# Performance work log

Measured on AMD Instinct MI355X. Metric: run time of the kernel, lower is better.

## Reference

```python
import jax, jax.numpy as jnp
import numpy as np


def binarize(t):
    # sign binarizer to exactly +/-1 (sign(0) -> +1), matching is_binary_tensor check
    return jnp.where(t >= 0, 1.0, -1.0).astype(t.dtype)


def setup_inputs() -> dict:
    key = jax.random.key(0)
    kx, kw, kb = jax.random.split(key, 3)
    x = jax.random.normal(kx, (32, 256, 56, 56), dtype=jnp.float32)
    weight = jax.random.normal(kw, (256, 256, 3, 3), dtype=jnp.float32)
    bias = jax.random.normal(kb, (256,), dtype=jnp.float32)
    return {"x": x, "weight": weight, "bias": bias}


def reference(x, weight, bias):
    bx = binarize(x)            # [B, Cin, H, W] in {-1, +1}
    bw = binarize(weight)       # [Cout, Cin, kh, kw] in {-1, +1}
    # F.conv2d(stride=1, padding=1, dilation=1, groups=1)
    out = jax.lax.conv_general_dilated(
        bx, bw,
        window_strides=(1, 1),
        padding=((1, 1), (1, 1)),
        dimension_numbers=("NCHW", "OIHW", "NCHW"),
    )
    return out + bias[None, :, None, None]
```

## Files before the change

kernel.cpp:

```cpp
#include <hip/hip_runtime.h>
#include <cstdint>

constexpr int B = 32, C = 256, H = 56, W = 56;
constexpr int HW = H * W;
constexpr int WORDS = C / 32;
constexpr int TAPS = 9;
constexpr int WPC = TAPS * WORDS;

__global__ __launch_bounds__(256) void pack_x_kernel(const float* __restrict__ x,
                                                     uint32_t* __restrict__ px) {
    int idx = blockIdx.x * 256 + threadIdx.x;
    if (idx >= B * HW) return;
    int b = idx / HW;
    int hw = idx - b * HW;
    const float* xp = x + (size_t)b * C * HW + hw;
    uint32_t words[WORDS];
    for (int wd = 0; wd < WORDS; ++wd) {
        uint32_t bits = 0;
        #pragma unroll
        for (int i = 0; i < 32; ++i) {
            bits |= (xp[(size_t)(wd * 32 + i) * HW] < 0.0f ? (1u << i) : 0u);
        }
        words[wd] = bits;
    }
    uint4* dst = reinterpret_cast<uint4*>(px + (size_t)idx * WORDS);
    dst[0] = make_uint4(words[0], words[1], words[2], words[3]);
    dst[1] = make_uint4(words[4], words[5], words[6], words[7]);
}

__global__ __launch_bounds__(256) void pack_w_kernel(const float* __restrict__ wt,
                                                     uint32_t* __restrict__ pw) {
    int idx = blockIdx.x * 256 + threadIdx.x;
    if (idx >= C * WPC) return;
    int co = idx / WPC;
    int r = idx - co * WPC;
    int tap = r / WORDS;
    int wd = r - tap * WORDS;
    const float* wp = wt + ((size_t)co * C + wd * 32) * TAPS + tap;
    uint32_t bits = 0;
    #pragma unroll
    for (int i = 0; i < 32; ++i)
        bits |= (wp[(size_t)i * TAPS] < 0.0f ? (1u << i) : 0u);
    pw[(size_t)co * WPC + (size_t)tap * WORDS + wd] = bits;
}

__global__ __launch_bounds__(64) void bconv_kernel(const uint32_t* __restrict__ px,
                                                   const uint32_t* __restrict__ pw,
                                                   const float* __restrict__ bias,
                                                   float* __restrict__ out) {
    const int lane = threadIdx.x;
    const int hw = blockIdx.x * 64 + lane;
    const int cobase = blockIdx.y * 64;
    const int b = blockIdx.z;
    const int h = hw / W;
    const int w = hw - h * W;

    uint32_t pxr[TAPS][WORDS];
    bool valid[TAPS];
    int nvalid = 0;
    #pragma unroll
    for (int dh = -1; dh <= 1; ++dh) {
        #pragma unroll
        for (int dw = -1; dw <= 1; ++dw) {
            const int t = (dh + 1) * 3 + (dw + 1);
            const int hh = h + dh, ww = w + dw;
            const bool v = (hh >= 0) & (hh < H) & (ww >= 0) & (ww < W);
            valid[t] = v;
            nvalid += v ? 1 : 0;
            if (v) {
                const uint4* p = reinterpret_cast<const uint4*>(
                    px + ((size_t)b * HW + (size_t)hh * W + ww) * WORDS);
                uint4 a = p[0], bq = p[1];
                pxr[t][0] = a.x;  pxr[t][1] = a.y;  pxr[t][2] = a.z;  pxr[t][3] = a.w;
                pxr[t][4] = bq.x; pxr[t][5] = bq.y; pxr[t][6] = bq.z; pxr[t][7] = bq.w;
            } else {
                #pragma unroll
                for (int k = 0; k < WORDS; ++k) pxr[t][k] = 0;
            }
        }
    }

    const float basef = (float)(256 * nvalid);
    float* op = out + ((size_t)b * C + cobase) * HW + hw;

    #pragma unroll 1
    for (int j = 0; j < 64; ++j) {
        const int co = cobase + j;
        const uint32_t* wrow = pw + (size_t)co * WPC;
        uint32_t total = 0;
        #pragma unroll
        for (int t = 0; t < TAPS; ++t) {
            uint32_t pt = 0;
            #pragma unroll
            for (int k = 0; k < WORDS; ++k)
                pt += __popc(pxr[t][k] ^ wrow[t * WORDS + k]);
            total += valid[t] ? pt : 0u;
        }
        float res = basef - 2.0f * (float)(int)total + bias[co];
        op[(size_t)j * HW] = res;
    }
}

extern "C" void kernel_launch(void* const* d_in, const int* in_sizes, int n_in,
                              void* d_out, int out_size, void* d_ws, size_t ws_size,
                              hipStream_t stream) {
    const float* x = (const float*)d_in[0];
    const float* wt = (const float*)d_in[1];
    const float* bias = (const float*)d_in[2];
    float* out = (float*)d_out;

    uint32_t* px = (uint32_t*)d_ws;
    uint32_t* pw = px + (size_t)B * HW * WORDS;

    pack_x_kernel<<<(B * HW + 255) / 256, 256, 0, stream>>>(x, px);
    pack_w_kernel<<<(C * WPC + 255) / 256, 256, 0, stream>>>(wt, pw);

    dim3 grid(HW / 64, C / 64, B);
    bconv_kernel<<<grid, 64, 0, stream>>>(px, pw, bias, out);
}
```

Baseline: 340.3 us.

## Pad packed activations, split border pixels into separate kernel, widen conv blocks

Packs activations into a zero-padded (58x58) bit layout, parallelized per word, so the main conv kernel loads all nine taps unconditionally and assumes every tap is valid, using a precomputed 2304+bias constant. A separate border kernel then recomputes and overwrites the 220 edge pixels per channel with the correct valid-tap count. The conv block grows to 256 threads covering all output channels, with four warps sharing one pixel set. Popcount accumulation is split into four independent chains. This adds an extra launch and computes edge pixels twice.

```diff
diff --git a/kernel.cpp b/kernel.cpp
--- a/kernel.cpp
+++ b/kernel.cpp
@@ -6,31 +6,32 @@
 constexpr int WORDS = C / 32;
 constexpr int TAPS = 9;
 constexpr int WPC = TAPS * WORDS;
+constexpr int PH = H + 2, PW = W + 2, PHW = PH * PW;
 
 __global__ __launch_bounds__(256) void pack_x_kernel(const float* __restrict__ x,
                                                      uint32_t* __restrict__ px) {
     int idx = blockIdx.x * 256 + threadIdx.x;
-    if (idx >= B * HW) return;
-    int b = idx / HW;
-    int hw = idx - b * HW;
-    const float* xp = x + (size_t)b * C * HW + hw;
-    uint32_t words[WORDS];
-    for (int wd = 0; wd < WORDS; ++wd) {
-        uint32_t bits = 0;
+    int pp = idx % PHW;
+    int r = idx / PHW;
+    int wd = r % WORDS;
+    int b = r / WORDS;
+    int ph = pp / PW, pwp = pp - ph * PW;
+    uint32_t bits = 0;
+    if (ph >= 1 && ph <= H && pwp >= 1 && pwp <= W) {
+        const float* xp = x + ((size_t)b * C + wd * 32) * HW + (size_t)(ph - 1) * W + (pwp - 1);
         #pragma unroll
-        for (int i = 0; i < 32; ++i) {
-            bits |= (xp[(size_t)(wd * 32 + i) * HW] < 0.0f ? (1u << i) : 0u);
-        }
-        words[wd] = bits;
+        for (int i = 0; i < 32; ++i)
+            bits |= (xp[(size_t)i * HW] < 0.0f ? (1u << i) : 0u);
     }
-    uint4* dst = reinterpret_cast<uint4*>(px + (size_t)idx * WORDS);
-    dst[0] = make_uint4(words[0], words[1], words[2], words[3]);
-    dst[1] = make_uint4(words[4], words[5], words[6], words[7]);
+    px[((size_t)(b * PH + ph) * PW + pwp) * WORDS + wd] = bits;
 }
 
 __global__ __launch_bounds__(256) void pack_w_kernel(const float* __restrict__ wt,
-                                                     uint32_t* __restrict__ pw) {
+                                                     const float* __restrict__ bias,
+                                                     uint32_t* __restrict__ pw,
+                                                     float* __restrict__ basep) {
     int idx = blockIdx.x * 256 + threadIdx.x;
+    if (idx < C) basep[idx] = 2304.0f + bias[idx];
     if (idx >= C * WPC) return;
     int co = idx / WPC;
     int r = idx - co * WPC;
@@ -44,19 +45,69 @@
     pw[(size_t)co * WPC + (size_t)tap * WORDS + wd] = bits;
 }
 
-__global__ __launch_bounds__(64) void bconv_kernel(const uint32_t* __restrict__ px,
-                                                   const uint32_t* __restrict__ pw,
-                                                   const float* __restrict__ bias,
-                                                   float* __restrict__ out) {
-    const int lane = threadIdx.x;
+__global__ __launch_bounds__(256) void bconv_kernel(const uint32_t* __restrict__ px,
+                                                    const uint32_t* __restrict__ pw,
+                                                    const float* __restrict__ basep,
+                                                    float* __restrict__ out) {
+    const int lane = threadIdx.x & 63;
+    const int wid = __builtin_amdgcn_readfirstlane(threadIdx.x >> 6);
     const int hw = blockIdx.x * 64 + lane;
-    const int cobase = blockIdx.y * 64;
-    const int b = blockIdx.z;
+    const int b = blockIdx.y;
     const int h = hw / W;
     const int w = hw - h * W;
 
     uint32_t pxr[TAPS][WORDS];
-    bool valid[TAPS];
+    #pragma unroll
+    for (int dh = -1; dh <= 1; ++dh) {
+        #pragma unroll
+        for (int dw = -1; dw <= 1; ++dw) {
+            const int t = (dh + 1) * 3 + (dw + 1);
+            const uint4* p = reinterpret_cast<const uint4*>(
+                px + ((size_t)(b * PH + (h + 1 + dh)) * PW + (w + 1 + dw)) * WORDS);
+            uint4 a = p[0], q = p[1];
+            pxr[t][0] = a.x; pxr[t][1] = a.y; pxr[t][2] = a.z; pxr[t][3] = a.w;
+            pxr[t][4] = q.x; pxr[t][5] = q.y; pxr[t][6] = q.z; pxr[t][7] = q.w;
+        }
+    }
+
+    const int cobase = wid * 64;
+    const uint32_t* wbase = pw + (size_t)cobase * WPC;
+    const float* bbase = basep + cobase;
+    float* op = out + ((size_t)b * C + cobase) * HW + hw;
+
+    #pragma unroll 1
+    for (int j = 0; j < 64; ++j) {
+        const uint32_t* wr = wbase + (size_t)j * WPC;
+        uint32_t acc[4] = {0u, 0u, 0u, 0u};
+        #pragma unroll
+        for (int t = 0; t < TAPS; ++t) {
+            #pragma unroll
+            for (int k = 0; k < WORDS; ++k)
+                acc[(t * WORDS + k) & 3] += __popc(pxr[t][k] ^ wr[t * WORDS + k]);
+        }
+        uint32_t total = (acc[0] + acc[1]) + (acc[2] + acc[3]);
+        float res = fmaf(-2.0f, (float)(int)total, bbase[j]);
+        op[(size_t)j * HW] = res;
+    }
+}
+
+__global__ __launch_bounds__(256) void border_kernel(const uint32_t* __restrict__ px,
+                                                     const uint32_t* __restrict__ pw,
+                                                     const float* __restrict__ bias,
+                                                     float* __restrict__ out) {
+    int idx = blockIdx.x * 256 + threadIdx.x;
+    int e = idx % 220;
+    int r = idx / 220;
+    int co = r & 255;
+    int b = r >> 8;
+    int h, w;
+    if (e < 56)       { h = 0;            w = e; }
+    else if (e < 112) { h = 55;           w = e - 56; }
+    else if (e < 166) { h = 1 + (e - 112); w = 0; }
+    else              { h = 1 + (e - 166); w = 55; }
+
+    const uint32_t* wr = pw + (size_t)co * WPC;
+    uint32_t total = 0;
     int nvalid = 0;
     #pragma unroll
     for (int dh = -1; dh <= 1; ++dh) {
@@ -65,40 +116,17 @@
             const int t = (dh + 1) * 3 + (dw + 1);
             const int hh = h + dh, ww = w + dw;
             const bool v = (hh >= 0) & (hh < H) & (ww >= 0) & (ww < W);
-            valid[t] = v;
-            nvalid += v ? 1 : 0;
-            if (v) {
-                const uint4* p = reinterpret_cast<const uint4*>(
-                    px + ((size_t)b * HW + (size_t)hh * W + ww) * WORDS);
-                uint4 a = p[0], bq = p[1];
-                pxr[t][0] = a.x;  pxr[t][1] = a.y;  pxr[t][2] = a.z;  pxr[t][3] = a.w;
-                pxr[t][4] = bq.x; pxr[t][5] = bq.y; pxr[t][6] = bq.z; pxr[t][7] = bq.w;
-            } else {
-                #pragma unroll
-                for (int k = 0; k < WORDS; ++k) pxr[t][k] = 0;
-            }
-        }
-    }
-
-    const float basef = (float)(256 * nvalid);
-    float* op = out + ((size_t)b * C + cobase) * HW + hw;
-
-    #pragma unroll 1
-    for (int j = 0; j < 64; ++j) {
-        const int co = cobase + j;
-        const uint32_t* wrow = pw + (size_t)co * WPC;
-        uint32_t total = 0;
-        #pragma unroll
-        for (int t = 0; t < TAPS; ++t) {
+            const uint32_t* p = px + ((size_t)(b * PH + (hh + 1)) * PW + (ww + 1)) * WORDS;
             uint32_t pt = 0;
             #pragma unroll
             for (int k = 0; k < WORDS; ++k)
-                pt += __popc(pxr[t][k] ^ wrow[t * WORDS + k]);
-            total += valid[t] ? pt : 0u;
+                pt += __popc(p[k] ^ wr[t * WORDS + k]);
+            total += v ? pt : 0u;
+            nvalid += v ? 1 : 0;
         }
-        float res = basef - 2.0f * (float)(int)total + bias[co];
-        op[(size_t)j * HW] = res;
     }
+    float res = (float)(256 * nvalid) - 2.0f * (float)(int)total + bias[co];
+    out[((size_t)b * C + co) * HW + (size_t)h * W + w] = res;
 }
 
 extern "C" void kernel_launch(void* const* d_in, const int* in_sizes, int n_in,
@@ -110,11 +138,14 @@
     float* out = (float*)d_out;
 
     uint32_t* px = (uint32_t*)d_ws;
-    uint32_t* pw = px + (size_t)B * HW * WORDS;
+    uint32_t* pw = px + (size_t)B * PHW * WORDS;
+    float* basep = (float*)(pw + (size_t)C * WPC);
 
-    pack_x_kernel<<<(B * HW + 255) / 256, 256, 0, stream>>>(x, px);
-    pack_w_kernel<<<(C * WPC + 255) / 256, 256, 0, stream>>>(wt, pw);
+    pack_x_kernel<<<(B * WORDS * PHW) / 256, 256, 0, stream>>>(x, px);
+    pack_w_kernel<<<(C * WPC + 255) / 256, 256, 0, stream>>>(wt, bias, pw, basep);
 
-    dim3 grid(HW / 64, C / 64, B);
-    bconv_kernel<<<grid, 64, 0, stream>>>(px, pw, bias, out);
+    dim3 grid(HW / 64, B);
+    bconv_kernel<<<grid, 256, 0, stream>>>(px, pw, basep, out);
+
+    border_kernel<<<(B * C * 220) / 256, 256, 0, stream>>>(px, pw, bias, out);
 }
```

Result: slower. 382.9 us (+12.5%).
